# Optimization experiments

Measured on AMD Instinct MI355X. Metric: run time of the kernel, lower is better.

Reference implementation:

```python
import jax, jax.numpy as jnp
import numpy as np

B, F, N = 32, 10, 512   # batch_num, win_size (all_feature), node_num
E = 8192                # edges per graph
INTER = 256             # GAT inter_dim
HEADS = 2
NEG_SLOPE = 0.2
BN_EPS = 1e-5


def setup_inputs() -> dict:
    key = jax.random.key(0)
    ks = jax.random.split(key, 16)
    data = jax.random.normal(ks[0], (B, F, N), dtype=jnp.float32)
    # loop-free random edges: src != dst (matches PyG remove_self_loops + add_self_loops)
    dst = jax.random.randint(ks[1], (E,), 0, N)
    off = jax.random.randint(ks[2], (E,), 1, N)
    src = (dst + off) % N
    org_edge_index = jnp.stack([src, dst]).astype(jnp.int64)
    g = 0.05
    return {
        "data": data,
        "org_edge_index": org_edge_index,
        "W1": jax.random.normal(ks[3], (F, HEADS * INTER), dtype=jnp.float32) * g,
        "as1": jax.random.normal(ks[4], (HEADS, INTER), dtype=jnp.float32) * g,
        "ad1": jax.random.normal(ks[5], (HEADS, INTER), dtype=jnp.float32) * g,
        "b1": jnp.zeros((HEADS * INTER,), dtype=jnp.float32),
        "W2": jax.random.normal(ks[6], (HEADS * INTER, HEADS * INTER), dtype=jnp.float32) * g,
        "as2": jax.random.normal(ks[7], (HEADS, INTER), dtype=jnp.float32) * g,
        "ad2": jax.random.normal(ks[8], (HEADS, INTER), dtype=jnp.float32) * g,
        "b2": jnp.zeros((HEADS * INTER,), dtype=jnp.float32),
        "Wfc": jax.random.normal(ks[9], (HEADS * INTER, 1), dtype=jnp.float32) * g,
        "bfc": jnp.zeros((1,), dtype=jnp.float32),
        "gamma": jnp.ones((1,), dtype=jnp.float32),
        "beta": jnp.zeros((1,), dtype=jnp.float32),
    }


def _gat_conv(x, src, dst, W, a_src, a_dst, b):
    # PyG GATConv (v1), concat=True, negative_slope=0.2
    n = x.shape[0]
    H, C = a_src.shape
    h = (x @ W).reshape(n, H, C)                       # [n, H, C]
    al_s = jnp.einsum('nhc,hc->nh', h, a_src)          # [n, H]
    al_d = jnp.einsum('nhc,hc->nh', h, a_dst)
    e = jax.nn.leaky_relu(al_s[src] + al_d[dst], NEG_SLOPE)  # [Etot, H]
    emax = jax.ops.segment_max(e, dst, num_segments=n)       # segment softmax over dst
    ex = jnp.exp(e - emax[dst])
    denom = jax.ops.segment_sum(ex, dst, num_segments=n)
    alpha = ex / (denom[dst] + 1e-16)                  # [Etot, H]
    msg = h[src] * alpha[:, :, None]                   # [Etot, H, C]
    out = jax.ops.segment_sum(msg, dst, num_segments=n)
    return out.reshape(n, H * C) + b


def reference(data, org_edge_index, W1, as1, ad1, b1, W2, as2, ad2, b2,
              Wfc, bfc, gamma, beta):
    b_num, feat, n_num = data.shape
    x = data.reshape(-1, feat)                         # faithful to x.view(-1, all_feature)
    total = b_num * n_num
    # batched edge index: repeat with per-batch node offsets
    offs = jnp.arange(b_num, dtype=org_edge_index.dtype) * n_num
    be = (org_edge_index[:, None, :] + offs[None, :, None]).reshape(2, -1)
    loops = jnp.arange(total, dtype=org_edge_index.dtype)  # add_self_loops
    src = jnp.concatenate([be[0], loops])
    dst = jnp.concatenate([be[1], loops])
    x1 = _gat_conv(x, src, dst, W1, as1, ad1, b1)      # dropout = identity (eval)
    x2 = _gat_conv(x1, src, dst, W2, as2, ad2, b2)
    y = x2 @ Wfc + bfc                                 # [total, 1]
    # BatchNorm1d(1), eval mode: running_mean=0, running_var=1
    y = y * (gamma / jnp.sqrt(1.0 + BN_EPS)) + beta
    y = jax.nn.relu(y)
    return y.reshape(-1, 1, n_num)                     # [B, 1, N]
```

## Files before the change

kernel.cpp:

```cpp
#include <hip/hip_runtime.h>
#include <math.h>

#define B_  32
#define F_  10
#define N_  512
#define E_  8192
#define T_  16384
#define EC_ 8704
#define HC_ 512
#define C_  256

typedef __attribute__((ext_vector_type(8))) short bf16x8;
typedef __attribute__((ext_vector_type(4))) float f32x4;
typedef __attribute__((ext_vector_type(2))) float f32x2;

__device__ __forceinline__ unsigned short f2bf(float f) {
    unsigned int u = __float_as_uint(f);
    u = (u + 0x7fffu + ((u >> 16) & 1u)) >> 16;
    return (unsigned short)u;
}
__device__ __forceinline__ float bf2f(unsigned short b) {
    return __uint_as_float(((unsigned int)b) << 16);
}
__device__ __forceinline__ float dot4(f32x4 a, f32x4 b) {
    f32x4 m = a * b;
    return m[0] + m[1] + m[2] + m[3];
}
__device__ __forceinline__ unsigned int pack2(unsigned short a, unsigned short b) {
    return (unsigned int)a | ((unsigned int)b << 16);
}
__device__ __forceinline__ f32x2 bfpair(unsigned int u) {
    f32x2 r;
    r[0] = __uint_as_float(u << 16);
    r[1] = __uint_as_float(u & 0xffff0000u);
    return r;
}
__device__ __forceinline__ void async_cp16(const void* g, void* l) {
    __builtin_amdgcn_global_load_lds(
        (const __attribute__((address_space(1))) unsigned int*)g,
        (__attribute__((address_space(3))) unsigned int*)l, 16, 0, 0);
}

__device__ __forceinline__ int node_map(int bid, int wid) {
    int x = bid & 7;
    int rest = bid >> 3;
    int batch = x * 4 + (rest >> 7);
    int within = rest & 127;
    return batch * 512 + within * 4 + wid;
}

__global__ __launch_bounds__(256) void gemm1_kernel(
    const float* __restrict__ X, const float* __restrict__ W1,
    const float* __restrict__ a_s, const float* __restrict__ a_d,
    unsigned short* __restrict__ Hs, float* __restrict__ als,
    float* __restrict__ ald, float* __restrict__ als2z,
    float* __restrict__ ald2z,
    const int* __restrict__ eidx, const float* __restrict__ W2,
    int* __restrict__ off0, int* __restrict__ csr0,
    unsigned short* __restrict__ Bhi, unsigned short* __restrict__ Blo) {
    __shared__ float shmem[1056];
    int tid = threadIdx.x;

    if (blockIdx.x >= 512) {
        if (blockIdx.x < 768) {
            int pb = blockIdx.x - 512;
            float* t = shmem;
            int bx = pb & 15, by = pb >> 4;
            int kb = bx * 32, nb = by * 32;
            int tx = tid & 31, ty = tid >> 5;
#pragma unroll
            for (int r = ty; r < 32; r += 8)
                t[r * 33 + tx] = W2[(size_t)(kb + r) * HC_ + nb + tx];
            __syncthreads();
#pragma unroll
            for (int r = ty; r < 32; r += 8) {
                float v = t[tx * 33 + r];
                unsigned short h = f2bf(v);
                Bhi[(size_t)(nb + r) * HC_ + kb + tx] = h;
                Blo[(size_t)(nb + r) * HC_ + kb + tx] = f2bf(v - bf2f(h));
            }
        } else {
            int* cnt = (int*)shmem;
            int* scn = (int*)shmem + 512;
            cnt[2 * tid] = 0; cnt[2 * tid + 1] = 0;
            __syncthreads();
            const int* edst = eidx + E_;
            for (int j = tid; j < EC_; j += 256) {
                int d = (j < E_) ? edst[j] : (j - E_);
                atomicAdd(&cnt[d], 1);
            }
            __syncthreads();
            int c0 = cnt[2 * tid], c1 = cnt[2 * tid + 1];
            scn[tid] = c0 + c1;
            __syncthreads();
            for (int d = 1; d < 256; d <<= 1) {
                int add = (tid >= d) ? scn[tid - d] : 0;
                __syncthreads();
                scn[tid] += add;
                __syncthreads();
            }
            int e0 = scn[tid] - (c0 + c1);
            off0[2 * tid] = e0;
            off0[2 * tid + 1] = e0 + c0;
            cnt[2 * tid] = e0;
            cnt[2 * tid + 1] = e0 + c0;
            if (tid == 255) off0[512] = EC_;
            __syncthreads();
            for (int j = tid; j < EC_; j += 256) {
                int s, d;
                if (j < E_) { s = eidx[j]; d = edst[j]; }
                else { s = d = j - E_; }
                int pos = atomicAdd(&cnt[d], 1);
                csr0[pos] = s;
            }
        }
        return;
    }

    float* xs = shmem;
    int lane = tid & 63, w = tid >> 6;
    int q = blockIdx.x;
    int batch = (q & 7) * 4 + (q >> 7);
    int sub = (q >> 3) & 15;
    int nb = batch * 512 + sub * 32 + w * 8;
    int col = lane * 8;

    f32x4 w1r[F_][2];
#pragma unroll
    for (int k = 0; k < F_; ++k) {
        w1r[k][0] = *(const f32x4*)&W1[k * HC_ + col];
        w1r[k][1] = *(const f32x4*)&W1[k * HC_ + col + 4];
    }
    f32x4 asl = *(const f32x4*)&a_s[col], ash = *(const f32x4*)&a_s[col + 4];
    f32x4 adl = *(const f32x4*)&a_d[col], adh = *(const f32x4*)&a_d[col + 4];

    const float* xp = X + (size_t)nb * F_;
    if (lane < 40) {
        xs[w * 80 + lane] = xp[lane];
        xs[w * 80 + lane + 40] = xp[lane + 40];
    }
    if (lane < 16) als2z[nb * 2 + lane] = 0.f;
    else if (lane >= 48) ald2z[nb * 2 + lane - 48] = 0.f;

#pragma unroll
    for (int n = 0; n < 8; ++n) {
        f32x4 h0 = {0.f, 0.f, 0.f, 0.f}, h1 = h0;
#pragma unroll
        for (int k = 0; k < F_; ++k) {
            float xv = xs[w * 80 + n * F_ + k];
            h0 += xv * w1r[k][0];
            h1 += xv * w1r[k][1];
        }
        int node = nb + n;
        uint4 uh;
        uh.x = pack2(f2bf(h0[0]), f2bf(h0[1]));
        uh.y = pack2(f2bf(h0[2]), f2bf(h0[3]));
        uh.z = pack2(f2bf(h1[0]), f2bf(h1[1]));
        uh.w = pack2(f2bf(h1[2]), f2bf(h1[3]));
        *(uint4*)&Hs[(size_t)node * HC_ + col] = uh;
        float ps = dot4(h0, asl) + dot4(h1, ash);
        float pd = dot4(h0, adl) + dot4(h1, adh);
#pragma unroll
        for (int m = 1; m <= 16; m <<= 1) {
            ps += __shfl_xor(ps, m);
            pd += __shfl_xor(pd, m);
        }
        if (lane == 0)  { als[node * 2 + 0] = ps; ald[node * 2 + 0] = pd; }
        if (lane == 32) { als[node * 2 + 1] = ps; ald[node * 2 + 1] = pd; }
    }
}

template <int MODE>
__global__ __launch_bounds__(256) void agg_kernel(
    const unsigned short* __restrict__ Hin, const float* __restrict__ als,
    const float* __restrict__ ald, const int* __restrict__ off0,
    const int* __restrict__ csr0, const float* __restrict__ bias,
    unsigned short* __restrict__ Ahi,
    const float* __restrict__ Wfc, const float* __restrict__ bfc,
    const float* __restrict__ gamma, const float* __restrict__ beta,
    float* __restrict__ out) {
    int tid = threadIdx.x, lane = tid & 63, wid = tid >> 6;
    int dst = node_map(blockIdx.x, wid);
    int bbase = dst & ~511;
    int dl = dst & 511;
    int beg = off0[dl], end = off0[dl + 1], deg = end - beg;
    float ad0 = ald[2 * dst], ad1 = ald[2 * dst + 1];
    int col = lane * 8;
    f32x2 A0 = {0.f, 0.f}, A1 = A0, A2 = A0, A3 = A0;

    if (deg <= 64) {
        float e0 = -1e30f, e1 = -1e30f;
        int sl = 0;
        if (lane < deg) {
            sl = csr0[beg + lane] + bbase;
            float a0 = als[2 * sl], a1 = als[2 * sl + 1];
            e0 = a0 + ad0; e0 = e0 > 0.f ? e0 : 0.2f * e0;
            e1 = a1 + ad1; e1 = e1 > 0.f ? e1 : 0.2f * e1;
        }
        float m0 = e0, m1 = e1;
#pragma unroll
        for (int m = 1; m < 64; m <<= 1) {
            m0 = fmaxf(m0, __shfl_xor(m0, m));
            m1 = fmaxf(m1, __shfl_xor(m1, m));
        }
        float x0 = (lane < deg) ? expf(e0 - m0) : 0.f;
        float x1 = (lane < deg) ? expf(e1 - m1) : 0.f;
        float d0 = x0, d1 = x1;
#pragma unroll
        for (int m = 1; m < 64; m <<= 1) {
            d0 += __shfl_xor(d0, m);
            d1 += __shfl_xor(d1, m);
        }
        float w0l = x0 / (d0 + 1e-16f);
        float w1l = x1 / (d1 + 1e-16f);
        int e = 0;
        for (; e + 2 <= deg; e += 2) {
            int s0 = __shfl(sl, e), s1 = __shfl(sl, e + 1);
            float wa0 = __shfl(w0l, e),     wb0 = __shfl(w1l, e);
            float wa1 = __shfl(w0l, e + 1), wb1 = __shfl(w1l, e + 1);
            float w0 = (lane < 32) ? wa0 : wb0;
            float w1 = (lane < 32) ? wa1 : wb1;
            uint4 h0 = *(const uint4*)(Hin + (size_t)s0 * HC_ + col);
            uint4 h1 = *(const uint4*)(Hin + (size_t)s1 * HC_ + col);
            f32x2 w0v = {w0, w0}, w1v = {w1, w1};
            A0 = __builtin_elementwise_fma(w0v, bfpair(h0.x), A0);
            A1 = __builtin_elementwise_fma(w0v, bfpair(h0.y), A1);
            A2 = __builtin_elementwise_fma(w0v, bfpair(h0.z), A2);
            A3 = __builtin_elementwise_fma(w0v, bfpair(h0.w), A3);
            A0 = __builtin_elementwise_fma(w1v, bfpair(h1.x), A0);
            A1 = __builtin_elementwise_fma(w1v, bfpair(h1.y), A1);
            A2 = __builtin_elementwise_fma(w1v, bfpair(h1.z), A2);
            A3 = __builtin_elementwise_fma(w1v, bfpair(h1.w), A3);
        }
        for (; e < deg; ++e) {
            int s = __shfl(sl, e);
            float wa = __shfl(w0l, e);
            float wb = __shfl(w1l, e);
            float w = (lane < 32) ? wa : wb;
            uint4 hv = *(const uint4*)(Hin + (size_t)s * HC_ + col);
            f32x2 wv = {w, w};
            A0 = __builtin_elementwise_fma(wv, bfpair(hv.x), A0);
            A1 = __builtin_elementwise_fma(wv, bfpair(hv.y), A1);
            A2 = __builtin_elementwise_fma(wv, bfpair(hv.z), A2);
            A3 = __builtin_elementwise_fma(wv, bfpair(hv.w), A3);
        }
    } else {
        float m0 = -1e30f, m1 = -1e30f;
        for (int k = beg + lane; k < end; k += 64) {
            int s = csr0[k] + bbase;
            float e0 = als[2 * s] + ad0; e0 = e0 > 0.f ? e0 : 0.2f * e0;
            float e1 = als[2 * s + 1] + ad1; e1 = e1 > 0.f ? e1 : 0.2f * e1;
            m0 = fmaxf(m0, e0);
            m1 = fmaxf(m1, e1);
        }
#pragma unroll
        for (int m = 1; m < 64; m <<= 1) {
            m0 = fmaxf(m0, __shfl_xor(m0, m));
            m1 = fmaxf(m1, __shfl_xor(m1, m));
        }
        float d0 = 0.f, d1 = 0.f;
        for (int k = beg + lane; k < end; k += 64) {
            int s = csr0[k] + bbase;
            float e0 = als[2 * s] + ad0; e0 = e0 > 0.f ? e0 : 0.2f * e0;
            float e1 = als[2 * s + 1] + ad1; e1 = e1 > 0.f ? e1 : 0.2f * e1;
            d0 += expf(e0 - m0);
            d1 += expf(e1 - m1);
        }
#pragma unroll
        for (int m = 1; m < 64; m <<= 1) {
            d0 += __shfl_xor(d0, m);
            d1 += __shfl_xor(d1, m);
        }
        float inv0 = 1.f / (d0 + 1e-16f);
        float inv1 = 1.f / (d1 + 1e-16f);
        for (int k = beg; k < end; ++k) {
            int s = csr0[k] + bbase;
            float e0 = als[2 * s] + ad0; e0 = e0 > 0.f ? e0 : 0.2f * e0;
            float e1 = als[2 * s + 1] + ad1; e1 = e1 > 0.f ? e1 : 0.2f * e1;
            float w0 = expf(e0 - m0) * inv0;
            float w1 = expf(e1 - m1) * inv1;
            float w = (lane < 32) ? w0 : w1;
            uint4 hv = *(const uint4*)(Hin + (size_t)s * HC_ + col);
            f32x2 wv = {w, w};
            A0 = __builtin_elementwise_fma(wv, bfpair(hv.x), A0);
            A1 = __builtin_elementwise_fma(wv, bfpair(hv.y), A1);
            A2 = __builtin_elementwise_fma(wv, bfpair(hv.z), A2);
            A3 = __builtin_elementwise_fma(wv, bfpair(hv.w), A3);
        }
    }

    A0 += *(const f32x2*)&bias[col];
    A1 += *(const f32x2*)&bias[col + 2];
    A2 += *(const f32x2*)&bias[col + 4];
    A3 += *(const f32x2*)&bias[col + 6];

    if (MODE == 0) {
        uint4 uh;
        uh.x = pack2(f2bf(A0[0]), f2bf(A0[1]));
        uh.y = pack2(f2bf(A1[0]), f2bf(A1[1]));
        uh.z = pack2(f2bf(A2[0]), f2bf(A2[1]));
        uh.w = pack2(f2bf(A3[0]), f2bf(A3[1]));
        *(uint4*)&Ahi[(size_t)dst * HC_ + col] = uh;
    } else {
        float y = 0.f;
        y = fmaf(A0[0], Wfc[col + 0], y); y = fmaf(A0[1], Wfc[col + 1], y);
        y = fmaf(A1[0], Wfc[col + 2], y); y = fmaf(A1[1], Wfc[col + 3], y);
        y = fmaf(A2[0], Wfc[col + 4], y); y = fmaf(A2[1], Wfc[col + 5], y);
        y = fmaf(A3[0], Wfc[col + 6], y); y = fmaf(A3[1], Wfc[col + 7], y);
#pragma unroll
        for (int m = 1; m < 64; m <<= 1) y += __shfl_xor(y, m);
        if (lane == 0) {
            y += bfc[0];
            y = y * (gamma[0] * rsqrtf(1.f + 1e-5f)) + beta[0];
            out[dst] = y > 0.f ? y : 0.f;
        }
    }
}

__global__ __launch_bounds__(512, 1) void gemm2_kernel(
    const unsigned short* __restrict__ Ahi,
    const unsigned short* __restrict__ Bhi, const unsigned short* __restrict__ Blo,
    unsigned short* __restrict__ H2,
    const float* __restrict__ as2, const float* __restrict__ ad2,
    float* __restrict__ als2, float* __restrict__ ald2) {
    __shared__ __align__(16) char smem[135168];
    const int tid = threadIdx.x, lane = tid & 63, wid = tid >> 6;
    const int wr = wid >> 1, wc = wid & 1;
    const int g = (blockIdx.x & 7) * 32 + (blockIdx.x >> 3);
    const int row0 = (g >> 2) * 256, col0 = (g & 3) * 128;
    const int lr = lane & 15, lk = lane >> 4;
    const int x7 = lr & 7;

    f32x4 acc[4][4] = {};

    const char* gsrc[8];
    int loff[8];
#pragma unroll
    for (int l = 0; l < 8; ++l) {
        int i = tid + l * 512;
        if (i < 2048) {
            int r = i >> 3, c = i & 7;
            gsrc[l] = (const char*)(Ahi + (size_t)(row0 + r) * HC_ + ((c ^ (r & 7)) << 3));
            loff[l] = i << 4;
        } else if (i < 3072) {
            int j = i - 2048, r = j >> 3, c = j & 7;
            gsrc[l] = (const char*)(Bhi + (size_t)(col0 + r) * HC_ + ((c ^ (r & 7)) << 3));
            loff[l] = 32768 + (j << 4);
        } else {
            int j = i - 3072, r = j >> 3, c = j & 7;
            gsrc[l] = (const char*)(Blo + (size_t)(col0 + r) * HC_ + ((c ^ (r & 7)) << 3));
            loff[l] = 49152 + (j << 4);
        }
    }
    char* lds0 = smem;

#pragma unroll
    for (int l = 0; l < 8; ++l) async_cp16(gsrc[l], lds0 + loff[l]);
    asm volatile("s_waitcnt vmcnt(0)" ::: "memory");
    __builtin_amdgcn_s_barrier();

    int cur = 0;
    for (int kt = 0; kt < 8; ++kt) {
        if (kt < 7) {
            char* dst = lds0 + ((cur ^ 1) << 16);
#pragma unroll
            for (int l = 0; l < 8; ++l)
                async_cp16(gsrc[l] + (size_t)(kt + 1) * 128, dst + loff[l]);
        }
        const char* base = lds0 + (cur << 16);
#pragma unroll
        for (int kk = 0; kk < 2; ++kk) {
            bf16x8 a[4], bh[4], bl[4];
            int cx = ((kk * 4 + lk) ^ x7) << 4;
#pragma unroll
            for (int m = 0; m < 4; ++m) {
                int ra = wr * 64 + m * 16 + lr;
                int rb = wc * 64 + m * 16 + lr;
                a[m]  = *(const bf16x8*)(base + ra * 128 + cx);
                bh[m] = *(const bf16x8*)(base + 32768 + rb * 128 + cx);
                bl[m] = *(const bf16x8*)(base + 49152 + rb * 128 + cx);
            }
#pragma unroll
            for (int m = 0; m < 4; ++m)
#pragma unroll
                for (int n = 0; n < 4; ++n) {
                    acc[m][n] = __builtin_amdgcn_mfma_f32_16x16x32_bf16(a[m], bh[n], acc[m][n], 0, 0, 0);
                    acc[m][n] = __builtin_amdgcn_mfma_f32_16x16x32_bf16(a[m], bl[n], acc[m][n], 0, 0, 0);
                }
        }
        asm volatile("s_waitcnt vmcnt(0)" ::: "memory");
        __builtin_amdgcn_s_barrier();
        cur ^= 1;
    }

    float* tb = (float*)smem;
#pragma unroll
    for (int m = 0; m < 4; ++m)
#pragma unroll
        for (int i = 0; i < 4; ++i) {
            int row = wr * 64 + m * 16 + lk * 4 + i;
#pragma unroll
            for (int n = 0; n < 4; ++n)
                tb[row * 132 + wc * 64 + n * 16 + lr] = acc[m][n][i];
        }
    __syncthreads();
    const int head = col0 >> 8;
    const float* a_s2 = as2 + head * C_ + (col0 & 255);
    const float* a_d2 = ad2 + head * C_ + (col0 & 255);
#pragma unroll
    for (int p = 0; p < 8; ++p) {
        int q = tid + p * 512;
        int row = q >> 4, cs = (q & 15) * 8;
        const float* v = &tb[row * 132 + cs];
        uint4 uh;
        uh.x = pack2(f2bf(v[0]), f2bf(v[1]));
        uh.y = pack2(f2bf(v[2]), f2bf(v[3]));
        uh.z = pack2(f2bf(v[4]), f2bf(v[5]));
        uh.w = pack2(f2bf(v[6]), f2bf(v[7]));
        *(uint4*)&H2[(size_t)(row0 + row) * HC_ + col0 + cs] = uh;
        float ps = 0.f, pd = 0.f;
#pragma unroll
        for (int j = 0; j < 8; ++j) {
            ps = fmaf(v[j], a_s2[cs + j], ps);
            pd = fmaf(v[j], a_d2[cs + j], pd);
        }
#pragma unroll
        for (int m = 1; m < 16; m <<= 1) {
            ps += __shfl_xor(ps, m);
            pd += __shfl_xor(pd, m);
        }
        if ((tid & 15) == 0) {
            atomicAdd(&als2[(row0 + row) * 2 + head], ps);
            atomicAdd(&ald2[(row0 + row) * 2 + head], pd);
        }
    }
}

extern "C" void kernel_launch(void* const* d_in, const int* in_sizes, int n_in,
                              void* d_out, int out_size, void* d_ws, size_t ws_size,
                              hipStream_t stream) {
    const float* data  = (const float*)d_in[0];
    const int*   eidx  = (const int*)d_in[1];
    const float* W1    = (const float*)d_in[2];
    const float* as1   = (const float*)d_in[3];
    const float* ad1   = (const float*)d_in[4];
    const float* b1    = (const float*)d_in[5];
    const float* W2    = (const float*)d_in[6];
    const float* as2   = (const float*)d_in[7];
    const float* ad2   = (const float*)d_in[8];
    const float* b2    = (const float*)d_in[9];
    const float* Wfc   = (const float*)d_in[10];
    const float* bfc   = (const float*)d_in[11];
    const float* gamma = (const float*)d_in[12];
    const float* beta  = (const float*)d_in[13];
    float* out = (float*)d_out;

    char* base = (char*)d_ws;
    size_t o = 0;
    auto take = [&](size_t bytes) {
        char* p = base + o;
        o = (o + bytes + 255) & ~(size_t)255;
        return p;
    };
    int*   off0 = (int*)take((size_t)(N_ + 1) * 4);
    int*   csr0 = (int*)take((size_t)EC_ * 4);
    float* als1 = (float*)take((size_t)T_ * 2 * 4);
    float* ald1 = (float*)take((size_t)T_ * 2 * 4);
    float* als2 = (float*)take((size_t)T_ * 2 * 4);
    float* ald2 = (float*)take((size_t)T_ * 2 * 4);
    unsigned short* hs1 = (unsigned short*)take((size_t)T_ * HC_ * 2);
    unsigned short* hs2 = (unsigned short*)take((size_t)T_ * HC_ * 2);
    unsigned short* Ahi = (unsigned short*)take((size_t)T_ * HC_ * 2);
    unsigned short* Bhi = (unsigned short*)take((size_t)HC_ * HC_ * 2);
    unsigned short* Blo = (unsigned short*)take((size_t)HC_ * HC_ * 2);

    gemm1_kernel<<<769, 256, 0, stream>>>(data, W1, as1, ad1, hs1, als1, ald1,
                                          als2, ald2, eidx, W2, off0, csr0,
                                          Bhi, Blo);
    agg_kernel<0><<<4096, 256, 0, stream>>>(hs1, als1, ald1, off0, csr0, b1,
                                            Ahi, nullptr, nullptr, nullptr,
                                            nullptr, nullptr);
    gemm2_kernel<<<256, 512, 0, stream>>>(Ahi, Bhi, Blo, hs2, as2, ad2, als2, ald2);
    agg_kernel<1><<<4096, 256, 0, stream>>>(hs2, als2, ald2, off0, csr0, b2,
                                            nullptr, Wfc, bfc, gamma,
                                            beta, out);
}
```

Baseline: 93.32 us.

## Deepen gemm2 pipeline to 4-stage with smaller K tiles and MFMA priority

Restructures the gemm2 main loop from a double-buffered 64-wide K tile into a 4-stage ring of 32-wide K tiles, keeping three loads in flight and waiting with partial vmcnt counts instead of draining all loads each iteration. The LDS swizzle is changed to match the narrower rows, and s_setprio is raised around the MFMA block. The aim is to hide global-to-LDS latency better. The cost is twice as many barriers, and the partial waitcnt values must exactly match the number of loads still outstanding.

Result: slower. 95.35 us (+2.2%).

```diff
diff --git a/kernel.cpp b/kernel.cpp
--- a/kernel.cpp
+++ b/kernel.cpp
@@ -329,69 +329,70 @@
     const int g = (blockIdx.x & 7) * 32 + (blockIdx.x >> 3);
     const int row0 = (g >> 2) * 256, col0 = (g & 3) * 128;
     const int lr = lane & 15, lk = lane >> 4;
-    const int x7 = lr & 7;
+    const int cswz = (lk ^ ((lr >> 1) & 3)) << 4;
 
     f32x4 acc[4][4] = {};
 
-    const char* gsrc[8];
-    int loff[8];
-#pragma unroll
-    for (int l = 0; l < 8; ++l) {
+    const char* gsrc[4];
+    int loff[4];
+#pragma unroll
+    for (int l = 0; l < 4; ++l) {
         int i = tid + l * 512;
-        if (i < 2048) {
-            int r = i >> 3, c = i & 7;
-            gsrc[l] = (const char*)(Ahi + (size_t)(row0 + r) * HC_ + ((c ^ (r & 7)) << 3));
-            loff[l] = i << 4;
-        } else if (i < 3072) {
-            int j = i - 2048, r = j >> 3, c = j & 7;
-            gsrc[l] = (const char*)(Bhi + (size_t)(col0 + r) * HC_ + ((c ^ (r & 7)) << 3));
-            loff[l] = 32768 + (j << 4);
-        } else {
-            int j = i - 3072, r = j >> 3, c = j & 7;
-            gsrc[l] = (const char*)(Blo + (size_t)(col0 + r) * HC_ + ((c ^ (r & 7)) << 3));
-            loff[l] = 49152 + (j << 4);
-        }
-    }
-    char* lds0 = smem;
-
-#pragma unroll
-    for (int l = 0; l < 8; ++l) async_cp16(gsrc[l], lds0 + loff[l]);
-    asm volatile("s_waitcnt vmcnt(0)" ::: "memory");
+        int r, c, reg;
+        const unsigned short* bp;
+        if (i < 1024)      { r = i >> 2;          c = i & 3; reg = 0;
+                             bp = Ahi + (size_t)(row0 + r) * HC_; }
+        else if (i < 1536) { int j = i - 1024; r = j >> 2; c = j & 3; reg = 16384;
+                             bp = Bhi + (size_t)(col0 + r) * HC_; }
+        else               { int j = i - 1536; r = j >> 2; c = j & 3; reg = 24576;
+                             bp = Blo + (size_t)(col0 + r) * HC_; }
+        int cs = c ^ ((r >> 1) & 3);
+        gsrc[l] = (const char*)(bp + cs * 8);
+        loff[l] = reg + ((i < 1024) ? i : (i & 511)) * 16;
+    }
+
+#pragma unroll
+    for (int t = 0; t < 3; ++t) {
+        char* dst = smem + t * 32768;
+#pragma unroll
+        for (int l = 0; l < 4; ++l)
+            async_cp16(gsrc[l] + (size_t)t * 64, dst + loff[l]);
+    }
+    asm volatile("s_waitcnt vmcnt(8)" ::: "memory");
     __builtin_amdgcn_s_barrier();
 
-    int cur = 0;
-    for (int kt = 0; kt < 8; ++kt) {
-        if (kt < 7) {
-            char* dst = lds0 + ((cur ^ 1) << 16);
-#pragma unroll
-            for (int l = 0; l < 8; ++l)
-                async_cp16(gsrc[l] + (size_t)(kt + 1) * 128, dst + loff[l]);
-        }
-        const char* base = lds0 + (cur << 16);
-#pragma unroll
-        for (int kk = 0; kk < 2; ++kk) {
-            bf16x8 a[4], bh[4], bl[4];
-            int cx = ((kk * 4 + lk) ^ x7) << 4;
-#pragma unroll
-            for (int m = 0; m < 4; ++m) {
-                int ra = wr * 64 + m * 16 + lr;
-                int rb = wc * 64 + m * 16 + lr;
-                a[m]  = *(const bf16x8*)(base + ra * 128 + cx);
-                bh[m] = *(const bf16x8*)(base + 32768 + rb * 128 + cx);
-                bl[m] = *(const bf16x8*)(base + 49152 + rb * 128 + cx);
+    for (int kt = 0; kt < 16; ++kt) {
+        if (kt <= 12) {
+            char* dst = smem + ((kt + 3) & 3) * 32768;
+#pragma unroll
+            for (int l = 0; l < 4; ++l)
+                async_cp16(gsrc[l] + (size_t)(kt + 3) * 64, dst + loff[l]);
+        }
+        const char* base = smem + (kt & 3) * 32768;
+        bf16x8 a[4], bh[4], bl[4];
+#pragma unroll
+        for (int m = 0; m < 4; ++m) {
+            int ra = wr * 64 + m * 16 + lr;
+            int rb = wc * 64 + m * 16 + lr;
+            a[m]  = *(const bf16x8*)(base + ra * 64 + cswz);
+            bh[m] = *(const bf16x8*)(base + 16384 + rb * 64 + cswz);
+            bl[m] = *(const bf16x8*)(base + 24576 + rb * 64 + cswz);
+        }
+        __builtin_amdgcn_s_setprio(1);
+#pragma unroll
+        for (int m = 0; m < 4; ++m)
+#pragma unroll
+            for (int n = 0; n < 4; ++n) {
+                acc[m][n] = __builtin_amdgcn_mfma_f32_16x16x32_bf16(a[m], bh[n], acc[m][n], 0, 0, 0);
+                acc[m][n] = __builtin_amdgcn_mfma_f32_16x16x32_bf16(a[m], bl[n], acc[m][n], 0, 0, 0);
             }
-#pragma unroll
-            for (int m = 0; m < 4; ++m)
-#pragma unroll
-                for (int n = 0; n < 4; ++n) {
-                    acc[m][n] = __builtin_amdgcn_mfma_f32_16x16x32_bf16(a[m], bh[n], acc[m][n], 0, 0, 0);
-                    acc[m][n] = __builtin_amdgcn_mfma_f32_16x16x32_bf16(a[m], bl[n], acc[m][n], 0, 0, 0);
-                }
-        }
-        asm volatile("s_waitcnt vmcnt(0)" ::: "memory");
-        __builtin_amdgcn_s_barrier();
-        cur ^= 1;
-    }
+        __builtin_amdgcn_s_setprio(0);
+        if (kt <= 12)      asm volatile("s_waitcnt vmcnt(8)" ::: "memory");
+        else if (kt == 13) asm volatile("s_waitcnt vmcnt(4)" ::: "memory");
+        else if (kt == 14) asm volatile("s_waitcnt vmcnt(0)" ::: "memory");
+        if (kt < 15) __builtin_amdgcn_s_barrier();
+    }
+    __syncthreads();
 
     float* tb = (float*)smem;
 #pragma unroll
```
